# Kernel tuning notes

Measured on AMD Instinct MI355X. Metric: run time of the kernel, lower is better.

## Reference

```python
import jax, jax.numpy as jnp
import numpy as np

B, T, C = 64, 1024, 32   # batch, seq_len, n_embd
H, D = 4, 8              # num_heads, head_size (H*D == C)


def setup_inputs() -> dict:
    key = jax.random.key(0)
    ks = jax.random.split(key, 6)
    s = 0.02  # init scale for weights
    x = jax.random.normal(ks[0], (B, T, C), dtype=jnp.float32)
    Wq = jax.random.normal(ks[1], (H, C, D), dtype=jnp.float32) * s
    Wk = jax.random.normal(ks[2], (H, C, D), dtype=jnp.float32) * s
    Wv = jax.random.normal(ks[3], (H, C, D), dtype=jnp.float32) * s
    Wproj = jax.random.normal(ks[4], (H * D, C), dtype=jnp.float32) * s
    bproj = jnp.zeros((C,), dtype=jnp.float32)
    return {"x": x, "Wq": Wq, "Wk": Wk, "Wv": Wv, "Wproj": Wproj, "bproj": bproj}


def reference(x, Wq, Wk, Wv, Wproj, bproj):
    # All heads batched into one einsum instead of a Python loop over Head modules.
    q = jnp.einsum('btc,hcd->bhtd', x, Wq)
    k = jnp.einsum('btc,hcd->bhtd', x, Wk)
    v = jnp.einsum('btc,hcd->bhtd', x, Wv)
    scale = D ** -0.5
    att = jnp.einsum('bhtd,bhsd->bhts', q, k) * scale  # [B,H,T,T]
    causal = jnp.tril(jnp.ones((T, T), dtype=bool))
    att = jnp.where(causal, att, jnp.float32(-1e9))
    att = jax.nn.softmax(att, axis=-1)  # dropout omitted (eval mode)
    o = jnp.einsum('bhts,bhsd->bhtd', att, v)
    o = o.transpose(0, 2, 1, 3).reshape(B, T, H * D)  # concat heads on last dim
    return o @ Wproj + bproj  # final proj; output dropout omitted (eval mode)
```

## Files before the change

### kernel.cpp

```cpp
#include <hip/hip_runtime.h>
#include <math.h>

static constexpr int Bb = 64, Tt = 1024, Cc = 32, Hh = 4, Dd = 8;
static constexpr float QSCALE = 0.51006973f;

typedef _Float16 h2  __attribute__((ext_vector_type(2)));
typedef _Float16 v4h __attribute__((ext_vector_type(4)));
typedef float  f32x4 __attribute__((ext_vector_type(4)));

__device__ __forceinline__ h2 pkrtz(float a, float b) {
  return __builtin_bit_cast(h2, __builtin_amdgcn_cvt_pkrtz(a, b));
}

__device__ __forceinline__ float fdot2(h2 a, h2 b, float c) {
#if __has_builtin(__builtin_amdgcn_fdot2)
  return __builtin_amdgcn_fdot2(a, b, c, false);
#else
  return fmaf((float)a.x, (float)b.x, fmaf((float)a.y, (float)b.y, c));
#endif
}

__device__ __forceinline__ float frcp(float x) {
#if __has_builtin(__builtin_amdgcn_rcpf)
  return __builtin_amdgcn_rcpf(x);
#else
  return 1.0f / x;
#endif
}

__device__ __forceinline__ float bperm_f32(int src_lane, float v) {
  return __builtin_bit_cast(float,
      __builtin_amdgcn_ds_bpermute(src_lane << 2, __builtin_bit_cast(int, v)));
}

__device__ __forceinline__ h2 exp2h2(h2 s) {
  const h2 A3 = {(_Float16)0.05550411f, (_Float16)0.05550411f};
  const h2 A2 = {(_Float16)0.24022651f, (_Float16)0.24022651f};
  const h2 A1 = {(_Float16)0.69314718f, (_Float16)0.69314718f};
  const h2 ONE = {(_Float16)1.0f, (_Float16)1.0f};
  h2 t = A3 * s + A2;
  t = t * s + A1;
  t = t * s + ONE;
  return t;
}

union U4 { uint4 u; h2 h[4]; };
union P2 { uint2 u; h2 h[2]; v4h v; };

__device__ __forceinline__ void chain_step(const P2& ak, const v4h& bv,
                                           const P2& bq, f32x4& o) {
  const f32x4 zero4 = {0.f, 0.f, 0.f, 0.f};
  f32x4 s = __builtin_amdgcn_mfma_f32_16x16x16f16(ak.v, bq.v, zero4, 0, 0, 0);
  h2 p0 = exp2h2(pkrtz(s[0], s[1]));
  h2 p1 = exp2h2(pkrtz(s[2], s[3]));
  P2 pf; pf.h[0] = p0; pf.h[1] = p1;
  o = __builtin_amdgcn_mfma_f32_16x16x16f16(pf.v, bv, o, 0, 0, 0);
}

__device__ __forceinline__ void chain_step_masked(const P2& ak, const v4h& bv,
                                                  const P2& bq, f32x4& o,
                                                  h2 km0, h2 km1) {
  const f32x4 zero4 = {0.f, 0.f, 0.f, 0.f};
  f32x4 s = __builtin_amdgcn_mfma_f32_16x16x16f16(ak.v, bq.v, zero4, 0, 0, 0);
  h2 p0 = exp2h2(pkrtz(s[0], s[1])) * km0;
  h2 p1 = exp2h2(pkrtz(s[2], s[3])) * km1;
  P2 pf; pf.h[0] = p0; pf.h[1] = p1;
  o = __builtin_amdgcn_mfma_f32_16x16x16f16(pf.v, bv, o, 0, 0, 0);
}

__global__ void fused_attn_kernel(
    const float* __restrict__ x, const float* __restrict__ Wq,
    const float* __restrict__ Wk, const float* __restrict__ Wv,
    ushort* __restrict__ og)
{
  __shared__ h2 wT[3][Dd][16];
  __shared__ __align__(16) ushort ks[Tt * Dd];
  __shared__ __align__(16) ushort vs[9 * 1032];
  __shared__ __align__(16) ushort qs[Tt * Dd];

  const int tid = threadIdx.x;
  const int bh = blockIdx.x & 255;
  const int g  = blockIdx.x >> 8;
  const int b = bh >> 2, h = bh & 3;

  if (tid < 384) {
    const int mat = tid >> 7, d = (tid >> 4) & 7, c2 = tid & 15;
    const float* W = (mat == 0) ? Wq : (mat == 1) ? Wk : Wv;
    const float w0 = W[(h * Cc + 2 * c2) * Dd + d];
    const float w1 = W[(h * Cc + 2 * c2 + 1) * Dd + d];
    wT[mat][d][c2] = pkrtz(w0, w1);
  } else if (tid < 512) {
    const int i = tid - 384;
    const unsigned one2 = 0x3C003C00u;
    *(uint4*)(vs + 8 * 1032 + i * 8) = make_uint4(one2, one2, one2, one2);
  }

  const int t = tid;
  h2 xr[16];
  {
    const float4* gx = (const float4*)(x + ((long)b * Tt + t) * Cc);
#pragma unroll
    for (int i = 0; i < 8; ++i) {
      float4 v = gx[i];
      xr[2 * i]     = pkrtz(v.x, v.y);
      xr[2 * i + 1] = pkrtz(v.z, v.w);
    }
  }
  __syncthreads();

#pragma unroll
  for (int mat = 0; mat < 3; ++mat) {
    float a[Dd];
#pragma unroll
    for (int d = 0; d < Dd; ++d) {
      float s = 0.f;
#pragma unroll
      for (int c2 = 0; c2 < 16; ++c2) s = fdot2(xr[c2], wT[mat][d][c2], s);
      a[d] = s;
    }
    if (mat == 2) {
#pragma unroll
      for (int d = 0; d < Dd; ++d)
        ((_Float16*)vs)[d * 1032 + t] = (_Float16)a[d];
    } else {
      const float sc = (mat == 0) ? QSCALE : 1.0f;
      ushort* dst = (mat == 0) ? qs : ks;
      U4 uu;
#pragma unroll
      for (int i = 0; i < 4; ++i)
        uu.h[i] = pkrtz(a[2 * i] * sc, a[2 * i + 1] * sc);
      ((uint4*)(dst + t * Dd))[0] = uu.u;
    }
  }
  __syncthreads();

  const int lane = tid & 63;
  const int u  = __builtin_amdgcn_readfirstlane(tid >> 6);
  const int W  = g * 16 + u;
  const int rb0 = W, rb1 = 63 - W;

  const int n = lane & 15, quad = lane >> 4;
  const ushort* kbase = ks + n * Dd + (quad & 1) * 4;
  const int vr = (n <= 8) ? n : (n - 8);
  const ushort* vbase = vs + vr * 1032 + quad * 4;

  const h2 km0 = {(_Float16)((4 * quad + 0) <= n ? 1.f : 0.f),
                  (_Float16)((4 * quad + 1) <= n ? 1.f : 0.f)};
  const h2 km1 = {(_Float16)((4 * quad + 2) <= n ? 1.f : 0.f),
                  (_Float16)((4 * quad + 3) <= n ? 1.f : 0.f)};

  P2 bq0, bq1;
  {
    uint2 r0 = *(const uint2*)(qs + (rb0 * 16 + n) * Dd + (quad & 1) * 4);
    uint2 r1 = *(const uint2*)(qs + (rb1 * 16 + n) * Dd + (quad & 1) * 4);
    if (quad & 2) { r0.x = 0; r0.y = 0; r1.x = 0; r1.y = 0; }
    bq0.u = r0; bq1.u = r1;
  }

  const f32x4 zero4 = {0.f, 0.f, 0.f, 0.f};
  f32x4 o0 = zero4, o1 = zero4;

#define LOAD_AKBV                                         \
  P2 ak; ak.u = *(const uint2*)(kbase + ct * 128);        \
  const v4h bv = *(const v4h*)(vbase + ct * 16);

  int ct = 0;
#pragma unroll 2
  for (; ct < rb0; ++ct) {
    LOAD_AKBV;
    chain_step(ak, bv, bq0, o0);
    chain_step(ak, bv, bq1, o1);
  }
  {
    LOAD_AKBV;
    chain_step_masked(ak, bv, bq0, o0, km0, km1);
    chain_step(ak, bv, bq1, o1);
    ++ct;
  }
#pragma unroll 2
  for (; ct < rb1; ++ct) {
    LOAD_AKBV;
    chain_step(ak, bv, bq1, o1);
  }
  {
    LOAD_AKBV;
    chain_step_masked(ak, bv, bq1, o1, km0, km1);
  }
#undef LOAD_AKBV

  const int lsrc = (lane & 48) | 8;
#pragma unroll
  for (int r = 0; r < 4; ++r) {
    const float l0 = bperm_f32(lsrc, o0[r]);
    const float ov0 = o0[r] * frcp(l0);
    const float l1 = bperm_f32(lsrc, o1[r]);
    const float ov1 = o1[r] * frcp(l1);
    if (n < 8) {
      const int q0 = rb0 * 16 + 4 * quad + r;
      const int q1 = rb1 * 16 + 4 * quad + r;
      ((_Float16*)og)[(((long)b * Tt + q0) * Hh + h) * Dd + n] = (_Float16)ov0;
      ((_Float16*)og)[(((long)b * Tt + q1) * Hh + h) * Dd + n] = (_Float16)ov1;
    }
  }
}

__global__ __launch_bounds__(256) void proj_kernel(
    const ushort* __restrict__ o_ws, const float* __restrict__ Wp,
    const float* __restrict__ bp, float* __restrict__ out)
{
  __shared__ h2 wT[Cc][16];
  __shared__ float bps[Cc];
  const int tid = threadIdx.x;
  {
    const int c = tid & 31, hp = tid >> 5;
#pragma unroll
    for (int i = 0; i < 2; ++i) {
      const int hd2 = hp + 8 * i;
      wT[c][hd2] = pkrtz(Wp[(2 * hd2) * Cc + c], Wp[(2 * hd2 + 1) * Cc + c]);
    }
    if (tid < Cc) bps[tid] = bp[tid];
  }
  __syncthreads();

  const int bt = blockIdx.x * 256 + tid;
  h2 orow[16];
  {
    const uint4* op = (const uint4*)(o_ws + (long)bt * Cc);
#pragma unroll
    for (int w = 0; w < 4; ++w) {
      U4 uu; uu.u = op[w];
#pragma unroll
      for (int i = 0; i < 4; ++i) orow[w * 4 + i] = uu.h[i];
    }
  }
  float acc[Cc];
#pragma unroll
  for (int c = 0; c < Cc; ++c) {
    float a = bps[c];
#pragma unroll
    for (int hd2 = 0; hd2 < 16; ++hd2) a = fdot2(orow[hd2], wT[c][hd2], a);
    acc[c] = a;
  }
  float4* og2 = (float4*)(out + (long)bt * Cc);
#pragma unroll
  for (int c4 = 0; c4 < 8; ++c4)
    og2[c4] = make_float4(acc[c4 * 4], acc[c4 * 4 + 1], acc[c4 * 4 + 2], acc[c4 * 4 + 3]);
}

extern "C" void kernel_launch(void* const* d_in, const int* in_sizes, int n_in,
                              void* d_out, int out_size, void* d_ws, size_t ws_size,
                              hipStream_t stream) {
  const float* x  = (const float*)d_in[0];
  const float* Wq = (const float*)d_in[1];
  const float* Wk = (const float*)d_in[2];
  const float* Wv = (const float*)d_in[3];
  const float* Wp = (const float*)d_in[4];
  const float* bp = (const float*)d_in[5];
  float* out = (float*)d_out;

  ushort* o_ws = (ushort*)d_ws;

  fused_attn_kernel<<<Bb * Hh * 2, 1024, 0, stream>>>(x, Wq, Wk, Wv, o_ws);
  proj_kernel<<<Bb * Tt / 256, 256, 0, stream>>>(o_ws, Wp, bp, out);
}
```

Measured before the change: 102.8 us.

## Split QKV projection into separate kernel and shrink attention blocks

```diff
diff --git a/kernel.cpp b/kernel.cpp
--- a/kernel.cpp
+++ b/kernel.cpp
@@ -68,78 +68,107 @@
   o = __builtin_amdgcn_mfma_f32_16x16x16f16(pf.v, bv, o, 0, 0, 0);
 }
 
-__global__ void fused_attn_kernel(
+__global__ void qkv_kernel(
     const float* __restrict__ x, const float* __restrict__ Wq,
     const float* __restrict__ Wk, const float* __restrict__ Wv,
-    ushort* __restrict__ og)
+    ushort* __restrict__ Qg, ushort* __restrict__ Kg, ushort* __restrict__ Vg)
 {
-  __shared__ h2 wT[3][Dd][16];
+  __shared__ h2 wT[3][Hh][Dd][17];
+
+  const int tid = threadIdx.x;
+  const int b = blockIdx.x >> 2, q = blockIdx.x & 3;
+  const int t = q * 256 + (tid >> 2);
+  const int h = tid & 3;
+
+  for (int e = tid; e < 1536; e += 1024) {
+    const int mat = e >> 9, r = e & 511;
+    const int hh = r >> 7, d = (r >> 4) & 7, c2 = r & 15;
+    const float* W = (mat == 0) ? Wq : (mat == 1) ? Wk : Wv;
+    const float w0 = W[(hh * Cc + 2 * c2) * Dd + d];
+    const float w1 = W[(hh * Cc + 2 * c2 + 1) * Dd + d];
+    wT[mat][hh][d][c2] = pkrtz(w0, w1);
+  }
+
+  h2 xr[16];
+  {
+    const float4* gx = (const float4*)(x + ((long)b * Tt + t) * Cc);
+#pragma unroll
+    for (int i = 0; i < 8; ++i) {
+      float4 v = gx[i];
+      xr[2 * i]     = pkrtz(v.x, v.y);
+      xr[2 * i + 1] = pkrtz(v.z, v.w);
+    }
+  }
+  __syncthreads();
+
+  const long bh = (long)(b * Hh + h);
+#pragma unroll
+  for (int mat = 0; mat < 3; ++mat) {
+    float a[Dd];
+#pragma unroll
+    for (int d = 0; d < Dd; ++d) {
+      float s = 0.f;
+#pragma unroll
+      for (int c2 = 0; c2 < 16; ++c2) s = fdot2(xr[c2], wT[mat][h][d][c2], s);
+      a[d] = s;
+    }
+    if (mat == 2) {
+#pragma unroll
+      for (int d = 0; d < Dd; ++d)
+        ((_Float16*)Vg)[bh * (Dd * Tt) + d * Tt + t] = (_Float16)a[d];
+    } else {
+      const float sc = (mat == 0) ? QSCALE : 1.0f;
+      ushort* dst = (mat == 0) ? Qg : Kg;
+      U4 uu;
+#pragma unroll
+      for (int i = 0; i < 4; ++i)
+        uu.h[i] = pkrtz(a[2 * i] * sc, a[2 * i + 1] * sc);
+      ((uint4*)(dst + (bh * Tt + t) * Dd))[0] = uu.u;
+    }
+  }
+}
+
+__global__ void attn_kernel(
+    const ushort* __restrict__ Qg, const ushort* __restrict__ Kg,
+    const ushort* __restrict__ Vg, ushort* __restrict__ og)
+{
   __shared__ __align__(16) ushort ks[Tt * Dd];
   __shared__ __align__(16) ushort vs[9 * 1032];
-  __shared__ __align__(16) ushort qs[Tt * Dd];
 
   const int tid = threadIdx.x;
   const int bh = blockIdx.x & 255;
   const int g  = blockIdx.x >> 8;
   const int b = bh >> 2, h = bh & 3;
 
-  if (tid < 384) {
-    const int mat = tid >> 7, d = (tid >> 4) & 7, c2 = tid & 15;
-    const float* W = (mat == 0) ? Wq : (mat == 1) ? Wk : Wv;
-    const float w0 = W[(h * Cc + 2 * c2) * Dd + d];
-    const float w1 = W[(h * Cc + 2 * c2 + 1) * Dd + d];
-    wT[mat][d][c2] = pkrtz(w0, w1);
-  } else if (tid < 512) {
-    const int i = tid - 384;
-    const unsigned one2 = 0x3C003C00u;
-    *(uint4*)(vs + 8 * 1032 + i * 8) = make_uint4(one2, one2, one2, one2);
-  }
-
-  const int t = tid;
-  h2 xr[16];
-  {
-    const float4* gx = (const float4*)(x + ((long)b * Tt + t) * Cc);
-#pragma unroll
-    for (int i = 0; i < 8; ++i) {
-      float4 v = gx[i];
-      xr[2 * i]     = pkrtz(v.x, v.y);
-      xr[2 * i + 1] = pkrtz(v.z, v.w);
-    }
-  }
-  __syncthreads();
-
-#pragma unroll
-  for (int mat = 0; mat < 3; ++mat) {
-    float a[Dd];
-#pragma unroll
-    for (int d = 0; d < Dd; ++d) {
-      float s = 0.f;
-#pragma unroll
-      for (int c2 = 0; c2 < 16; ++c2) s = fdot2(xr[c2], wT[mat][d][c2], s);
-      a[d] = s;
-    }
-    if (mat == 2) {
-#pragma unroll
-      for (int d = 0; d < Dd; ++d)
-        ((_Float16*)vs)[d * 1032 + t] = (_Float16)a[d];
-    } else {
-      const float sc = (mat == 0) ? QSCALE : 1.0f;
-      ushort* dst = (mat == 0) ? qs : ks;
-      U4 uu;
-#pragma unroll
-      for (int i = 0; i < 4; ++i)
-        uu.h[i] = pkrtz(a[2 * i] * sc, a[2 * i + 1] * sc);
-      ((uint4*)(dst + t * Dd))[0] = uu.u;
-    }
-  }
-  __syncthreads();
-
   const int lane = tid & 63;
   const int u  = __builtin_amdgcn_readfirstlane(tid >> 6);
-  const int W  = g * 16 + u;
+  const int W  = g * 8 + u;
   const int rb0 = W, rb1 = 63 - W;
-
   const int n = lane & 15, quad = lane >> 4;
+
+  const ushort* Qbh = Qg + (long)bh * (Tt * Dd);
+  uint2 r0 = *(const uint2*)(Qbh + (rb0 * 16 + n) * Dd + (quad & 1) * 4);
+  uint2 r1 = *(const uint2*)(Qbh + (rb1 * 16 + n) * Dd + (quad & 1) * 4);
+
+  {
+    const uint4* Ksrc = (const uint4*)(Kg + (long)bh * (Tt * Dd));
+    const uint4* Vsrc = (const uint4*)(Vg + (long)bh * (Tt * Dd));
+    uint4* kd = (uint4*)ks;
+    uint4* vd = (uint4*)vs;
+#pragma unroll
+    for (int i = 0; i < 2; ++i) {
+      const int idx = tid + i * 512;
+      kd[idx] = Ksrc[idx];
+      const int d = idx >> 7, c = idx & 127;
+      vd[d * 129 + c] = Vsrc[idx];
+    }
+    if (tid < 128) {
+      const unsigned one2 = 0x3C003C00u;
+      vd[1032 + tid] = make_uint4(one2, one2, one2, one2);
+    }
+  }
+  __syncthreads();
+
   const ushort* kbase = ks + n * Dd + (quad & 1) * 4;
   const int vr = (n <= 8) ? n : (n - 8);
   const ushort* vbase = vs + vr * 1032 + quad * 4;
@@ -150,12 +179,8 @@
                   (_Float16)((4 * quad + 3) <= n ? 1.f : 0.f)};
 
   P2 bq0, bq1;
-  {
-    uint2 r0 = *(const uint2*)(qs + (rb0 * 16 + n) * Dd + (quad & 1) * 4);
-    uint2 r1 = *(const uint2*)(qs + (rb1 * 16 + n) * Dd + (quad & 1) * 4);
-    if (quad & 2) { r0.x = 0; r0.y = 0; r1.x = 0; r1.y = 0; }
-    bq0.u = r0; bq1.u = r1;
-  }
+  if (quad & 2) { r0.x = 0; r0.y = 0; r1.x = 0; r1.y = 0; }
+  bq0.u = r0; bq1.u = r1;
 
   const f32x4 zero4 = {0.f, 0.f, 0.f, 0.f};
   f32x4 o0 = zero4, o1 = zero4;
@@ -208,7 +233,7 @@
     const ushort* __restrict__ o_ws, const float* __restrict__ Wp,
     const float* __restrict__ bp, float* __restrict__ out)
 {
-  __shared__ h2 wT[Cc][16];
+  __shared__ h2 wT[Cc][17];
   __shared__ float bps[Cc];
   const int tid = threadIdx.x;
   {
@@ -222,7 +247,8 @@
   }
   __syncthreads();
 
-  const int bt = blockIdx.x * 256 + tid;
+  const int bt = blockIdx.x * 64 + (tid >> 2);
+  const int cq = tid & 3;
   h2 orow[16];
   {
     const uint4* op = (const uint4*)(o_ws + (long)bt * Cc);
@@ -233,18 +259,18 @@
       for (int i = 0; i < 4; ++i) orow[w * 4 + i] = uu.h[i];
     }
   }
-  float acc[Cc];
-#pragma unroll
-  for (int c = 0; c < Cc; ++c) {
+  float acc[8];
+#pragma unroll
+  for (int j = 0; j < 8; ++j) {
+    const int c = cq * 8 + j;
     float a = bps[c];
 #pragma unroll
     for (int hd2 = 0; hd2 < 16; ++hd2) a = fdot2(orow[hd2], wT[c][hd2], a);
-    acc[c] = a;
-  }
-  float4* og2 = (float4*)(out + (long)bt * Cc);
-#pragma unroll
-  for (int c4 = 0; c4 < 8; ++c4)
-    og2[c4] = make_float4(acc[c4 * 4], acc[c4 * 4 + 1], acc[c4 * 4 + 2], acc[c4 * 4 + 3]);
+    acc[j] = a;
+  }
+  float4* og2 = (float4*)(out + (long)bt * Cc + cq * 8);
+  og2[0] = make_float4(acc[0], acc[1], acc[2], acc[3]);
+  og2[1] = make_float4(acc[4], acc[5], acc[6], acc[7]);
 }
 
 extern "C" void kernel_launch(void* const* d_in, const int* in_sizes, int n_in,
@@ -259,7 +285,11 @@
   float* out = (float*)d_out;
 
   ushort* o_ws = (ushort*)d_ws;
-
-  fused_attn_kernel<<<Bb * Hh * 2, 1024, 0, stream>>>(x, Wq, Wk, Wv, o_ws);
-  proj_kernel<<<Bb * Tt / 256, 256, 0, stream>>>(o_ws, Wp, bp, out);
-}
+  ushort* Qg = (ushort*)d_ws + 2097152;
+  ushort* Kg = Qg + 2097152;
+  ushort* Vg = Kg + 2097152;
+
+  qkv_kernel<<<Bb * 4, 1024, 0, stream>>>(x, Wq, Wk, Wv, Qg, Kg, Vg);
+  attn_kernel<<<Bb * Hh * 4, 512, 0, stream>>>(Qg, Kg, Vg, o_ws);
+  proj_kernel<<<Bb * Tt / 64, 256, 0, stream>>>(o_ws, Wp, bp, out);
+}
```

Result: no change. 102.1 us (-0.6%).
